# Kernel tuning notes

Hardware: AMD Instinct MI355X
Metric: run time of the kernel (lower is better)

Reference implementation:

```python
import jax, jax.numpy as jnp
import numpy as np

N_NODES = 50000
N_EDGES = 600000
HIDDEN = 128
N_FEAT = 1
N_CLASSES = 2
N_GRAPHS = 500


def gcn_conv(x, W, b, src, dst, n_nodes):
    # PyG GCNConv: add self-loops, symmetric normalization deg^{-1/2} A_hat deg^{-1/2}, then XW + b
    h = x @ W  # [N, out]
    deg = jnp.zeros((n_nodes,), h.dtype).at[dst].add(1.0) + 1.0  # +1 for self-loop
    dinv = jax.lax.rsqrt(deg)
    norm = dinv[src] * dinv[dst]  # [E]
    agg = jax.ops.segment_sum(h[src] * norm[:, None], dst, num_segments=n_nodes)
    # self-loop contribution: norm_ii = dinv_i^2
    agg = agg + h * (dinv * dinv)[:, None]
    return agg + b


def setup_inputs() -> dict:
    key = jax.random.key(0)
    ks = jax.random.split(key, 12)
    x = jax.random.normal(ks[0], (N_NODES, N_FEAT), dtype=jnp.float32)
    edge_index = jax.random.randint(ks[1], (2, N_EDGES), 0, N_NODES, dtype=jnp.int64)
    batch = jnp.sort(jax.random.randint(ks[2], (N_NODES,), 0, N_GRAPHS, dtype=jnp.int64))

    def glorot(k, fan_in, fan_out):
        lim = np.sqrt(6.0 / (fan_in + fan_out)).astype(np.float32)
        return jax.random.uniform(k, (fan_in, fan_out), jnp.float32, -lim, lim)

    W1 = glorot(ks[3], N_FEAT, HIDDEN)
    b1 = jnp.zeros((HIDDEN,), jnp.float32)
    W2 = glorot(ks[4], HIDDEN, HIDDEN)
    b2 = jnp.zeros((HIDDEN,), jnp.float32)
    W3 = glorot(ks[5], HIDDEN, HIDDEN)
    b3 = jnp.zeros((HIDDEN,), jnp.float32)
    Wlin = glorot(ks[6], HIDDEN, N_CLASSES)
    blin = jnp.zeros((N_CLASSES,), jnp.float32)
    return {"x": x, "W1": W1, "b1": b1, "W2": W2, "b2": b2, "W3": W3,
            "b3": b3, "Wlin": Wlin, "blin": blin,
            "edge_index": edge_index, "batch": batch}


def reference(x, W1, b1, W2, b2, W3, b3, Wlin, blin, edge_index, batch):
    src, dst = edge_index[0], edge_index[1]
    n = x.shape[0]
    h = jax.nn.relu(gcn_conv(x, W1, b1, src, dst, n))
    h = jax.nn.relu(gcn_conv(h, W2, b2, src, dst, n))
    h = gcn_conv(h, W3, b3, src, dst, n)
    # global mean pool over graphs
    sums = jax.ops.segment_sum(h, batch, num_segments=N_GRAPHS)
    counts = jax.ops.segment_sum(jnp.ones((n,), h.dtype), batch, num_segments=N_GRAPHS)
    pooled = sums / jnp.maximum(counts, 1.0)[:, None]  # [G, HIDDEN]
    # dropout is identity in eval mode
    return pooled @ Wlin + blin  # [G, N_CLASSES]
```

## Files before the change

kernel.cpp:

```cpp
#include <hip/hip_runtime.h>

#define N_NODES 50000
#define N_EDGES 600000
#define HID     128
#define NG      500
#define MAXDEG  48
#define NEB     147
#define NBUCK   782
#define BCAP    1024

typedef __attribute__((ext_vector_type(8))) short short8;
typedef __attribute__((ext_vector_type(4))) float f32x4;

static __device__ __forceinline__ ushort f2bf(float f) {
    uint u = __float_as_uint(f);
    return (ushort)((u + 0x7fffu + ((u >> 16) & 1u)) >> 16);
}
static __device__ __forceinline__ float bf2f(ushort h) {
    return __uint_as_float(((uint)h) << 16);
}


__global__ __launch_bounds__(256) void k_bin(const int* __restrict__ src,
                                             const int* __restrict__ dst,
                                             int* __restrict__ gcnt,
                                             uint* __restrict__ ebuf,
                                             const float* __restrict__ W2,
                                             const float* __restrict__ W3,
                                             const float* __restrict__ Wlin,
                                             const float* __restrict__ b3,
                                             const float* __restrict__ blin,
                                             const int* __restrict__ batch,
                                             float* __restrict__ w3buf,
                                             ushort* __restrict__ w2fh,
                                             ushort* __restrict__ w2fl,
                                             int* __restrict__ starts) {
    if (blockIdx.x >= NEB) {
        int t = threadIdx.x;
        if (blockIdx.x == NEB) {
            int k = t >> 1, j = t & 1;
            float acc = 0.f;
            for (int m = 0; m < 128; m++) acc += W3[k * 128 + m] * Wlin[m * 2 + j];
            w3buf[k * 2 + j] = acc;
            if (t < 2) {
                float c = 0.f;
                for (int m = 0; m < 128; m++) c += b3[m] * Wlin[m * 2 + t];
                w3buf[256 + t] = c + blin[t];
                w3buf[258 + t] = blin[t];
            }
            for (int g = t; g <= NG; g += 256) {
                int lo = 0, hi = N_NODES;
                while (lo < hi) { int mid = (lo + hi) >> 1; if (batch[mid] < g) lo = mid + 1; else hi = mid; }
                starts[g] = lo;
            }
        } else {
            int q = blockIdx.x - (NEB + 1);
            for (int idx = q * 4096 + t; idx < (q + 1) * 4096; idx += 256) {
                int nt = idx >> 11, kt = (idx >> 9) & 3, ln = (idx >> 3) & 63, i = idx & 7;
                int k = kt * 32 + (ln >> 4) * 8 + i;
                int col = nt * 16 + (ln & 15);
                float v = W2[k * 128 + col];
                ushort h = f2bf(v);
                w2fh[idx] = h;
                w2fl[idx] = f2bf(v - bf2f(h));
            }
        }
        return;
    }
    __shared__ int lcnt[NBUCK];
    __shared__ int gbase[NBUCK];
    int t = threadIdx.x;
    for (int i = t; i < NBUCK; i += 256) lcnt[i] = 0;
    __syncthreads();
    uint pk[16];
    uint blp[16];
    const int4* s4 = (const int4*)src;
    const int4* d4 = (const int4*)dst;
    int b4 = blockIdx.x * 1024;
    #pragma unroll
    for (int u = 0; u < 4; u++) {
        int i4 = b4 + u * 256 + t;
        if (i4 < N_EDGES / 4) {
            int4 dv = d4[i4], sv = s4[i4];
            int dd[4] = {dv.x, dv.y, dv.z, dv.w};
            int ss[4] = {sv.x, sv.y, sv.z, sv.w};
            #pragma unroll
            for (int j = 0; j < 4; j++) {
                int b = dd[j] >> 6;
                int p = atomicAdd(&lcnt[b], 1);
                pk[u * 4 + j]  = ((uint)ss[j] << 16) | (uint)(dd[j] & 63);
                blp[u * 4 + j] = ((uint)b << 12) | (uint)p;
            }
        } else {
            #pragma unroll
            for (int j = 0; j < 4; j++) blp[u * 4 + j] = 0xFFFFFFFFu;
        }
    }
    __syncthreads();
    for (int i = t; i < NBUCK; i += 256) {
        int c = lcnt[i];
        gbase[i] = c ? atomicAdd(&gcnt[i], c) : 0;
    }
    __syncthreads();
    #pragma unroll
    for (int u = 0; u < 16; u++) {
        if (blp[u] != 0xFFFFFFFFu) {
            int b = (int)(blp[u] >> 12);
            int slot = gbase[b] + (int)(blp[u] & 0xFFFu);
            if (slot < BCAP) ebuf[b * BCAP + slot] = pk[u];
        }
    }
}


__global__ __launch_bounds__(256) void k_place(const int* __restrict__ gcnt,
                                               const uint* __restrict__ ebuf,
                                               const float* __restrict__ x,
                                               int* __restrict__ ell,
                                               int* __restrict__ cnt,
                                               float* __restrict__ dinv,
                                               float* __restrict__ xd) {
    int b = blockIdx.x;
    __shared__ int lc[64];
    int t = threadIdx.x;
    if (t < 64) lc[t] = 0;
    __syncthreads();
    int n = min(gcnt[b], BCAP);
    int d0 = b << 6;
    for (int i = t; i < n; i += 256) {
        uint e = ebuf[b * BCAP + i];
        int dl = (int)(e & 63u);
        int p = atomicAdd(&lc[dl], 1);
        if (p < MAXDEG) ell[(d0 + dl) * MAXDEG + p] = (int)(e >> 16);
    }
    __syncthreads();
    if (t < 64) {
        int d = d0 + t;
        if (d < N_NODES) {
            int c = lc[t];
            cnt[d] = c;
            float di = rsqrtf((float)c + 1.0f);
            dinv[d] = di;
            xd[d] = x[d] * di;
        }
    }
}

__global__ void k_s1d(const float* __restrict__ xd, const float* __restrict__ dinv,
                      const int* __restrict__ cnt, const int* __restrict__ ell,
                      float2* __restrict__ s1d) {
    int tid = blockIdx.x * 256 + threadIdx.x;
    int i = tid >> 3, sub = tid & 7;
    if (i >= N_NODES) return;
    int c = min(cnt[i], MAXDEG);
    float acc = 0.f;
    for (int p = sub; p < c; p += 8) acc += xd[ell[i * MAXDEG + p]];
    acc += __shfl_xor(acc, 1);
    acc += __shfl_xor(acc, 2);
    acc += __shfl_xor(acc, 4);
    if (sub == 0) {
        float di = dinv[i];
        float2 r = {(xd[i] + acc) * di, di};
        s1d[i] = r;
    }
}


__global__ __launch_bounds__(256) void k_h1(const float2* __restrict__ s1d,
                                            const int* __restrict__ cnt,
                                            const int* __restrict__ ell,
                                            const float* __restrict__ W1,
                                            const float* __restrict__ b1,
                                            ushort* __restrict__ hhi,
                                            ushort* __restrict__ hlo) {
    __shared__ float w1s[128], b1s[128];
    int t = threadIdx.x;
    if (t < 128) { w1s[t] = W1[t]; b1s[t] = b1[t]; }
    __syncthreads();
    int tid = blockIdx.x * 256 + t;
    int i = tid >> 3, sub = tid & 7;
    if (i >= N_NODES) return;
    float w1r[16], b1r[16];
    #pragma unroll
    for (int kk = 0; kk < 16; kk++) { w1r[kk] = w1s[sub * 16 + kk]; b1r[kk] = b1s[sub * 16 + kk]; }
    float2 sd = s1d[i];
    float di = sd.y;
    float ga[16];
    #pragma unroll
    for (int kk = 0; kk < 16; kk++) ga[kk] = fmaxf(sd.x * w1r[kk] + b1r[kk], 0.f) * (di * di);
    int c = min(cnt[i], MAXDEG);
    const int* row = &ell[i * MAXDEG];
    int p = 0;
    for (; p + 3 < c; p += 4) {
        int j0 = row[p], j1 = row[p + 1], j2 = row[p + 2], j3 = row[p + 3];
        float2 s0 = s1d[j0], s1v = s1d[j1], s2 = s1d[j2], s3 = s1d[j3];
        float wj0 = s0.y * di, wj1 = s1v.y * di, wj2 = s2.y * di, wj3 = s3.y * di;
        #pragma unroll
        for (int kk = 0; kk < 16; kk++) {
            ga[kk] += fmaxf(s0.x  * w1r[kk] + b1r[kk], 0.f) * wj0
                    + fmaxf(s1v.x * w1r[kk] + b1r[kk], 0.f) * wj1
                    + fmaxf(s2.x  * w1r[kk] + b1r[kk], 0.f) * wj2
                    + fmaxf(s3.x  * w1r[kk] + b1r[kk], 0.f) * wj3;
        }
    }
    for (; p < c; p++) {
        float2 sj = s1d[row[p]];
        float wj = sj.y * di;
        #pragma unroll
        for (int kk = 0; kk < 16; kk++)
            ga[kk] += fmaxf(sj.x * w1r[kk] + b1r[kk], 0.f) * wj;
    }
    uint h[8], lo[8];
    #pragma unroll
    for (int kk = 0; kk < 16; kk += 2) {
        ushort h0 = f2bf(ga[kk]);      ushort l0 = f2bf(ga[kk]     - bf2f(h0));
        ushort h1v = f2bf(ga[kk + 1]); ushort l1v = f2bf(ga[kk + 1] - bf2f(h1v));
        h[kk >> 1]  = (uint)h0 | ((uint)h1v << 16);
        lo[kk >> 1] = (uint)l0 | ((uint)l1v << 16);
    }
    uint4* ph = (uint4*)&hhi[i * 128 + sub * 16];
    ph[0] = make_uint4(h[0], h[1], h[2], h[3]);
    ph[1] = make_uint4(h[4], h[5], h[6], h[7]);
    uint4* pl = (uint4*)&hlo[i * 128 + sub * 16];
    pl[0] = make_uint4(lo[0], lo[1], lo[2], lo[3]);
    pl[1] = make_uint4(lo[4], lo[5], lo[6], lo[7]);
}


__global__ __launch_bounds__(256, 4) void k_gemm2(const ushort* __restrict__ hhi,
                                                  const ushort* __restrict__ hlo,
                                                  const ushort* __restrict__ w2fh,
                                                  const ushort* __restrict__ w2fl,
                                                  const float* __restrict__ b2,
                                                  const float* __restrict__ w3buf,
                                                  const float* __restrict__ dinv,
                                                  float* __restrict__ zd) {
    __shared__ float zpart[4 * 64 * 2];
    int t = threadIdx.x;
    int r0 = blockIdx.x * 64;
    int wv = t >> 6, l = t & 63, l15 = l & 15, lk = l >> 4;
    const short8* Bh = (const short8*)w2fh;
    const short8* Bl = (const short8*)w2fl;
    f32x4 acc[4][2];
    #pragma unroll
    for (int mt = 0; mt < 4; mt++)
        #pragma unroll
        for (int nt = 0; nt < 2; nt++) acc[mt][nt] = (f32x4){0.f, 0.f, 0.f, 0.f};
    #pragma unroll
    for (int kt = 0; kt < 4; kt++) {
        short8 bh0 = Bh[((2 * wv) * 4 + kt) * 64 + l];
        short8 bl0 = Bl[((2 * wv) * 4 + kt) * 64 + l];
        short8 bh1 = Bh[((2 * wv + 1) * 4 + kt) * 64 + l];
        short8 bl1 = Bl[((2 * wv + 1) * 4 + kt) * 64 + l];
        #pragma unroll
        for (int mt = 0; mt < 4; mt++) {
            int row = min(r0 + mt * 16 + l15, N_NODES - 1);
            int off = row * 128 + kt * 32 + lk * 8;
            short8 ah = *(const short8*)&hhi[off];
            short8 al = *(const short8*)&hlo[off];
            acc[mt][0] = __builtin_amdgcn_mfma_f32_16x16x32_bf16(ah, bh0, acc[mt][0], 0, 0, 0);
            acc[mt][0] = __builtin_amdgcn_mfma_f32_16x16x32_bf16(ah, bl0, acc[mt][0], 0, 0, 0);
            acc[mt][0] = __builtin_amdgcn_mfma_f32_16x16x32_bf16(al, bh0, acc[mt][0], 0, 0, 0);
            acc[mt][1] = __builtin_amdgcn_mfma_f32_16x16x32_bf16(ah, bh1, acc[mt][1], 0, 0, 0);
            acc[mt][1] = __builtin_amdgcn_mfma_f32_16x16x32_bf16(ah, bl1, acc[mt][1], 0, 0, 0);
            acc[mt][1] = __builtin_amdgcn_mfma_f32_16x16x32_bf16(al, bh1, acc[mt][1], 0, 0, 0);
        }
    }
    int cg0 = (2 * wv) * 16 + l15, cg1 = (2 * wv + 1) * 16 + l15;
    float b20 = b2[cg0], w00 = w3buf[cg0 * 2], w10 = w3buf[cg0 * 2 + 1];
    float b21 = b2[cg1], w01 = w3buf[cg1 * 2], w11 = w3buf[cg1 * 2 + 1];
    #pragma unroll
    for (int mt = 0; mt < 4; mt++) {
        #pragma unroll
        for (int r = 0; r < 4; r++) {
            float v0 = fmaxf(acc[mt][0][r] + b20, 0.f);
            float v1 = fmaxf(acc[mt][1][r] + b21, 0.f);
            float q0 = v0 * w00 + v1 * w01;
            float q1 = v0 * w10 + v1 * w11;
            #pragma unroll
            for (int o = 1; o < 16; o <<= 1) {
                q0 += __shfl_xor(q0, o);
                q1 += __shfl_xor(q1, o);
            }
            if (l15 == 0) {
                int rl = mt * 16 + lk * 4 + r;
                zpart[(wv * 64 + rl) * 2 + 0] = q0;
                zpart[(wv * 64 + rl) * 2 + 1] = q1;
            }
        }
    }
    __syncthreads();
    if (t < 128) {
        int rl = t >> 1, o = t & 1;
        float s = zpart[rl * 2 + o] + zpart[(64 + rl) * 2 + o]
                + zpart[(128 + rl) * 2 + o] + zpart[(192 + rl) * 2 + o];
        int rg = r0 + rl;
        if (rg < N_NODES) zd[rg * 2 + o] = s * dinv[rg];
    }
}


__global__ void k_aggz(const float* __restrict__ zd, const int* __restrict__ cnt,
                       const int* __restrict__ ell, const float* __restrict__ dinv,
                       const int* __restrict__ batch, float* __restrict__ gsum) {
    __shared__ float sa0[32], sa1[32];
    __shared__ int sg[32];
    int tid = blockIdx.x * 256 + threadIdx.x;
    int t = threadIdx.x;
    int i = tid >> 3, sub = tid & 7;
    const float2* Z = (const float2*)zd;
    float a0 = 0.f, a1 = 0.f;
    if (i < N_NODES) {
        int c = min(cnt[i], MAXDEG);
        for (int p = sub; p < c; p += 8) {
            float2 zj = Z[ell[i * MAXDEG + p]];
            a0 += zj.x; a1 += zj.y;
        }
    }
    a0 += __shfl_xor(a0, 1); a1 += __shfl_xor(a1, 1);
    a0 += __shfl_xor(a0, 2); a1 += __shfl_xor(a1, 2);
    a0 += __shfl_xor(a0, 4); a1 += __shfl_xor(a1, 4);
    if (sub == 0) {
        int li = t >> 3;
        if (i < N_NODES) {
            float di = dinv[i];
            float2 zi = Z[i];
            sa0[li] = (zi.x + a0) * di;
            sa1[li] = (zi.y + a1) * di;
            sg[li] = batch[i];
        } else { sa0[li] = 0.f; sa1[li] = 0.f; sg[li] = -1; }
    }
    __syncthreads();
    if (t < 32) {
        float v0 = sa0[t], v1 = sa1[t];
        int g = sg[t];
        #pragma unroll
        for (int o = 1; o < 32; o <<= 1) {
            float u0 = __shfl_up(v0, o), u1 = __shfl_up(v1, o);
            int ug = __shfl_up(g, o);
            if (t >= o && ug == g) { v0 += u0; v1 += u1; }
        }
        int gn = __shfl_down(g, 1);
        bool last = (t == 31) || (g != gn);
        if (last && g >= 0) {
            atomicAdd(&gsum[g * 2 + 0], v0);
            atomicAdd(&gsum[g * 2 + 1], v1);
        }
    }
}


__global__ __launch_bounds__(256) void k_final2(const float* __restrict__ gsum,
                                                const int* __restrict__ starts,
                                                const float* __restrict__ w3buf,
                                                float* __restrict__ out) {
    int t = threadIdx.x;
    for (int g = t; g < NG; g += 256) {
        int c = starts[g + 1] - starts[g];
        if (c > 0) {
            float inv = 1.0f / (float)c;
            out[g * 2 + 0] = gsum[g * 2 + 0] * inv + w3buf[256];
            out[g * 2 + 1] = gsum[g * 2 + 1] * inv + w3buf[257];
        } else {
            out[g * 2 + 0] = w3buf[258];
            out[g * 2 + 1] = w3buf[259];
        }
    }
}


extern "C" void kernel_launch(void* const* d_in, const int* in_sizes, int n_in,
                              void* d_out, int out_size, void* d_ws, size_t ws_size,
                              hipStream_t stream) {
    const float* x    = (const float*)d_in[0];
    const float* W1   = (const float*)d_in[1];
    const float* b1   = (const float*)d_in[2];
    const float* W2   = (const float*)d_in[3];
    const float* b2   = (const float*)d_in[4];
    const float* W3   = (const float*)d_in[5];
    const float* b3   = (const float*)d_in[6];
    const float* Wlin = (const float*)d_in[7];
    const float* blin = (const float*)d_in[8];
    const int*   eidx = (const int*)d_in[9];
    const int*   batch= (const int*)d_in[10];
    const int* esrc = eidx;
    const int* edst = eidx + N_EDGES;
    float* out = (float*)d_out;

    char* w = (char*)d_ws;
    size_t off = 0;
    auto alloc = [&](size_t bytes) { size_t o = off; off = (off + bytes + 255) & ~(size_t)255; return o; };
    int*   cnt    = (int*)  (w + alloc(N_NODES * 4));
    int*   ell    = (int*)  (w + alloc((size_t)N_NODES * MAXDEG * 4));
    float* dinv   = (float*)(w + alloc(N_NODES * 4));
    float* xd     = (float*)(w + alloc(N_NODES * 4));
    float2* s1d   = (float2*)(w + alloc((size_t)N_NODES * 8));
    float* w3buf  = (float*)(w + alloc(260 * 4));
    float* zd     = (float*)(w + alloc((size_t)N_NODES * 2 * 4));
    ushort* w2fh  = (ushort*)(w + alloc(16384 * 2));
    ushort* w2fl  = (ushort*)(w + alloc(16384 * 2));
    ushort* hhi   = (ushort*)(w + alloc((size_t)N_NODES * 128 * 2));
    ushort* hlo   = (ushort*)(w + alloc((size_t)N_NODES * 128 * 2));
    int*   starts = (int*)  (w + alloc((NG + 4) * 4));
    int*   gcnt   = (int*)  (w + alloc(1024 * 4));
    float* gsum   = (float*)(w + alloc(NG * 2 * 4));
    uint*  ebuf   = (uint*) (w + alloc((size_t)NBUCK * BCAP * 4));

    const int QB = (N_NODES * 8 + 255) / 256;
    hipMemsetAsync(gcnt, 0, 1024 * 4 + NG * 2 * 4, stream);
    k_bin<<<NEB + 5, 256, 0, stream>>>(esrc, edst, gcnt, ebuf, W2, W3, Wlin, b3, blin,
                                       batch, w3buf, w2fh, w2fl, starts);
    k_place<<<NBUCK, 256, 0, stream>>>(gcnt, ebuf, x, ell, cnt, dinv, xd);
    k_s1d<<<QB, 256, 0, stream>>>(xd, dinv, cnt, ell, s1d);
    k_h1<<<QB, 256, 0, stream>>>(s1d, cnt, ell, W1, b1, hhi, hlo);
    k_gemm2<<<NBUCK, 256, 0, stream>>>(hhi, hlo, w2fh, w2fl, b2, w3buf, dinv, zd);
    k_aggz<<<QB, 256, 0, stream>>>(zd, cnt, ell, dinv, batch, gsum);
    k_final2<<<1, 256, 0, stream>>>(gsum, starts, w3buf, out);
}
```

Measured before the change: 160.1 us.

## Split k_h1 neighbor loop across two half-warps with 32 threads per node

Reassigns k_h1 from 8 threads per node (16 features each) to 32 threads per node: 16 feature groups of 8, and two halves that each process alternate neighbors, combined with a shuffle-xor reduction. Neighbor loads are software-prefetched one iteration ahead, and launch bounds now request higher occupancy. The goal is more parallelism and shorter per-thread dependency chains when hiding gather latency. In exchange, four times as many threads are launched, the row indices and s1d values are loaded redundantly across feature groups, and half the lanes sit idle during the store.

```diff
diff --git a/kernel.cpp b/kernel.cpp
--- a/kernel.cpp
+++ b/kernel.cpp
@@ -166,64 +166,63 @@
 }
 
 
-__global__ __launch_bounds__(256) void k_h1(const float2* __restrict__ s1d,
-                                            const int* __restrict__ cnt,
-                                            const int* __restrict__ ell,
-                                            const float* __restrict__ W1,
-                                            const float* __restrict__ b1,
-                                            ushort* __restrict__ hhi,
-                                            ushort* __restrict__ hlo) {
+__global__ __launch_bounds__(256, 8) void k_h1(const float2* __restrict__ s1d,
+                                               const int* __restrict__ cnt,
+                                               const int* __restrict__ ell,
+                                               const float* __restrict__ W1,
+                                               const float* __restrict__ b1,
+                                               ushort* __restrict__ hhi,
+                                               ushort* __restrict__ hlo) {
     __shared__ float w1s[128], b1s[128];
     int t = threadIdx.x;
     if (t < 128) { w1s[t] = W1[t]; b1s[t] = b1[t]; }
     __syncthreads();
     int tid = blockIdx.x * 256 + t;
-    int i = tid >> 3, sub = tid & 7;
+    int i = tid >> 5;
+    int sub = t & 31;
+    int g = sub & 15;
+    int h = sub >> 4;
     if (i >= N_NODES) return;
-    float w1r[16], b1r[16];
-    #pragma unroll
-    for (int kk = 0; kk < 16; kk++) { w1r[kk] = w1s[sub * 16 + kk]; b1r[kk] = b1s[sub * 16 + kk]; }
+    float w1r[8], b1r[8];
+    #pragma unroll
+    for (int kk = 0; kk < 8; kk++) { w1r[kk] = w1s[g * 8 + kk]; b1r[kk] = b1s[g * 8 + kk]; }
     float2 sd = s1d[i];
     float di = sd.y;
-    float ga[16];
-    #pragma unroll
-    for (int kk = 0; kk < 16; kk++) ga[kk] = fmaxf(sd.x * w1r[kk] + b1r[kk], 0.f) * (di * di);
+    float ga[8];
+    #pragma unroll
+    for (int kk = 0; kk < 8; kk++)
+        ga[kk] = h ? 0.f : fmaxf(sd.x * w1r[kk] + b1r[kk], 0.f) * (di * di);
     int c = min(cnt[i], MAXDEG);
     const int* row = &ell[i * MAXDEG];
-    int p = 0;
-    for (; p + 3 < c; p += 4) {
-        int j0 = row[p], j1 = row[p + 1], j2 = row[p + 2], j3 = row[p + 3];
-        float2 s0 = s1d[j0], s1v = s1d[j1], s2 = s1d[j2], s3 = s1d[j3];
-        float wj0 = s0.y * di, wj1 = s1v.y * di, wj2 = s2.y * di, wj3 = s3.y * di;
+    int p = h;
+    if (p < c) {
+        float2 s = s1d[row[p]];
+        for (p += 2;; p += 2) {
+            bool more = (p < c);
+            float2 sn;
+            if (more) sn = s1d[row[p]];
+            float wj = s.y * di;
+            #pragma unroll
+            for (int kk = 0; kk < 8; kk++)
+                ga[kk] += fmaxf(s.x * w1r[kk] + b1r[kk], 0.f) * wj;
+            if (!more) break;
+            s = sn;
+        }
+    }
+    #pragma unroll
+    for (int kk = 0; kk < 8; kk++) ga[kk] += __shfl_xor(ga[kk], 16);
+    if (h == 0) {
+        uint hv[4], lv[4];
         #pragma unroll
-        for (int kk = 0; kk < 16; kk++) {
-            ga[kk] += fmaxf(s0.x  * w1r[kk] + b1r[kk], 0.f) * wj0
-                    + fmaxf(s1v.x * w1r[kk] + b1r[kk], 0.f) * wj1
-                    + fmaxf(s2.x  * w1r[kk] + b1r[kk], 0.f) * wj2
-                    + fmaxf(s3.x  * w1r[kk] + b1r[kk], 0.f) * wj3;
-        }
-    }
-    for (; p < c; p++) {
-        float2 sj = s1d[row[p]];
-        float wj = sj.y * di;
-        #pragma unroll
-        for (int kk = 0; kk < 16; kk++)
-            ga[kk] += fmaxf(sj.x * w1r[kk] + b1r[kk], 0.f) * wj;
-    }
-    uint h[8], lo[8];
-    #pragma unroll
-    for (int kk = 0; kk < 16; kk += 2) {
-        ushort h0 = f2bf(ga[kk]);      ushort l0 = f2bf(ga[kk]     - bf2f(h0));
-        ushort h1v = f2bf(ga[kk + 1]); ushort l1v = f2bf(ga[kk + 1] - bf2f(h1v));
-        h[kk >> 1]  = (uint)h0 | ((uint)h1v << 16);
-        lo[kk >> 1] = (uint)l0 | ((uint)l1v << 16);
-    }
-    uint4* ph = (uint4*)&hhi[i * 128 + sub * 16];
-    ph[0] = make_uint4(h[0], h[1], h[2], h[3]);
-    ph[1] = make_uint4(h[4], h[5], h[6], h[7]);
-    uint4* pl = (uint4*)&hlo[i * 128 + sub * 16];
-    pl[0] = make_uint4(lo[0], lo[1], lo[2], lo[3]);
-    pl[1] = make_uint4(lo[4], lo[5], lo[6], lo[7]);
+        for (int kk = 0; kk < 8; kk += 2) {
+            ushort h0 = f2bf(ga[kk]);      ushort l0 = f2bf(ga[kk]     - bf2f(h0));
+            ushort h1v = f2bf(ga[kk + 1]); ushort l1v = f2bf(ga[kk + 1] - bf2f(h1v));
+            hv[kk >> 1] = (uint)h0 | ((uint)h1v << 16);
+            lv[kk >> 1] = (uint)l0 | ((uint)l1v << 16);
+        }
+        *(uint4*)&hhi[i * 128 + g * 8] = make_uint4(hv[0], hv[1], hv[2], hv[3]);
+        *(uint4*)&hlo[i * 128 + g * 8] = make_uint4(lv[0], lv[1], lv[2], lv[3]);
+    }
 }
 
 
@@ -406,13 +405,14 @@
     float* gsum   = (float*)(w + alloc(NG * 2 * 4));
     uint*  ebuf   = (uint*) (w + alloc((size_t)NBUCK * BCAP * 4));
 
-    const int QB = (N_NODES * 8 + 255) / 256;
+    const int QB  = (N_NODES * 8 + 255) / 256;
+    const int QB2 = (N_NODES * 32 + 255) / 256;
     hipMemsetAsync(gcnt, 0, 1024 * 4 + NG * 2 * 4, stream);
     k_bin<<<NEB + 5, 256, 0, stream>>>(esrc, edst, gcnt, ebuf, W2, W3, Wlin, b3, blin,
                                        batch, w3buf, w2fh, w2fl, starts);
     k_place<<<NBUCK, 256, 0, stream>>>(gcnt, ebuf, x, ell, cnt, dinv, xd);
     k_s1d<<<QB, 256, 0, stream>>>(xd, dinv, cnt, ell, s1d);
-    k_h1<<<QB, 256, 0, stream>>>(s1d, cnt, ell, W1, b1, hhi, hlo);
+    k_h1<<<QB2, 256, 0, stream>>>(s1d, cnt, ell, W1, b1, hhi, hlo);
     k_gemm2<<<NBUCK, 256, 0, stream>>>(hhi, hlo, w2fh, w2fl, b2, w3buf, dinv, zd);
     k_aggz<<<QB, 256, 0, stream>>>(zd, cnt, ell, dinv, batch, gsum);
     k_final2<<<1, 256, 0, stream>>>(gsum, starts, w3buf, out);
```

Measured after the change: 164.5 us. 1.03x slower.
